# Kernel optimization log

Measured on AMD Instinct MI355X. Metric: run time of the kernel, lower is better.

Reference implementation:

```python
import jax, jax.numpy as jnp
import numpy as np

HEADS = 4
CHANNEL = 96
SCALE = CHANNEL ** (-0.5)


def setup_inputs() -> dict:
    key = jax.random.key(0)
    ks = jax.random.split(key, 6)
    x = jax.random.normal(ks[0], (64, 96, 112, 112), dtype=jnp.float32)
    z = jax.random.normal(ks[1], (64, 6, 192), dtype=jnp.float32)
    Wq = jax.random.normal(ks[2], (192, HEADS * CHANNEL), dtype=jnp.float32) * 0.02
    bq = jax.random.normal(ks[3], (HEADS * CHANNEL,), dtype=jnp.float32) * 0.02
    Wo = jax.random.normal(ks[4], (HEADS * CHANNEL, 192), dtype=jnp.float32) * 0.02
    bo = jax.random.normal(ks[5], (192,), dtype=jnp.float32) * 0.02
    return {"x": x, "z": z, "Wq": Wq, "bq": bq, "Wo": Wo, "bo": bo}


def reference(x, z, Wq, bq, Wo, bo):
    b, c, h, w = x.shape
    _, m, d = z.shape
    # flatten spatial: (b, hw, c)
    xf = x.reshape(b, c, h * w).transpose(0, 2, 1)
    # q: (b, heads, m, c)
    q = (z @ Wq + bq).reshape(b, m, HEADS, c).transpose(0, 2, 1, 3)
    # scores: (b, heads, m, hw); K = V = xf shared across heads
    dots = jnp.einsum('bhmc,bnc->bhmn', q, xf) * SCALE
    attn = jax.nn.softmax(dots, axis=-1)
    out = jnp.einsum('bhmn,bnc->bhmc', attn, xf)
    # rearrange b h m c -> b m (h c)
    out = out.transpose(0, 2, 1, 3).reshape(b, m, HEADS * c)
    return z + out @ Wo + bo
```

## Files before the change

### kernel.cpp

```cpp
#include <hip/hip_runtime.h>

#define BB 64
#define NHEADS 4
#define MM 6
#define RR 24
#define CC 96
#define NN 12544
#define DD 192
#define NC 128
#define TCH 7
#define NGRP 14
#define QSCALE 0.10206207261596577f

typedef __attribute__((ext_vector_type(8))) short short8;
typedef __attribute__((ext_vector_type(4))) float float4v;

__device__ __forceinline__ ushort f2b(float f) {
    union { float f; unsigned int u; } v; v.f = f;
    unsigned int u = v.u;
    unsigned int r = (u + 0x7FFFu + ((u >> 16) & 1u)) >> 16;
    return (ushort)r;
}

__global__ __launch_bounds__(256) void kA(const float* __restrict__ z,
                                          const float* __restrict__ Wq,
                                          const float* __restrict__ bq,
                                          ushort* __restrict__ Qg,
                                          float* __restrict__ Oacc,
                                          float* __restrict__ sacc) {
    __shared__ float zl[MM * DD];
    int t = threadIdx.x;
    int b = blockIdx.x / 3;
    int rg = blockIdx.x % 3;
    for (int i = t; i < MM * DD; i += 256) zl[i] = z[(size_t)b * MM * DD + i];
    for (int i = t; i < 768; i += 256) Oacc[(size_t)b * RR * CC + rg * 768 + i] = 0.f;
    if (rg == 0 && t < RR) sacc[b * RR + t] = 0.f;
    __syncthreads();
    #pragma unroll
    for (int i = 0; i < 3; ++i) {
        int idx = t + i * 256;
        int rr = idx / CC;
        int ch = idx - rr * CC;
        int r = rg * 8 + rr;
        int h = r / MM, m = r - h * MM;
        int col = h * CC + ch;
        float acc = bq[col];
        #pragma unroll 4
        for (int k = 0; k < DD; ++k)
            acc += zl[m * DD + k] * Wq[(size_t)k * (NHEADS * CC) + col];
        Qg[((size_t)b * RR + r) * CC + ch] = f2b(acc * QSCALE);
    }
}

__global__ __launch_bounds__(256, 4) void kB(const float* __restrict__ x,
                                             const ushort* __restrict__ Qg,
                                             float* __restrict__ Oacc,
                                             float* __restrict__ sacc) {
    __shared__ ushort xs[CC * NC];
    __shared__ ushort es[32 * NC];
    __shared__ ushort Qs[32 * 104];
    __shared__ float sdenL[RR];

    int t = threadIdx.x;
    int b = blockIdx.x / NGRP;
    int grp = blockIdx.x - b * NGRP;
    int w = t >> 6, lane = t & 63, q = lane >> 4, l15 = lane & 15;

    for (int i = t; i < 32 * 104; i += 256) Qs[i] = 0;
    __syncthreads();
    for (int i = t; i < RR * CC; i += 256) {
        int r = i / CC, ch = i - r * CC;
        Qs[r * 104 + ch] = Qg[((size_t)b * RR + r) * CC + ch];
    }
    if (t < RR) sdenL[t] = 0.f;

    int rt2 = w & 1;
    int ct0 = (w >> 1) * 3;
    float4v oacc0 = {0.f,0.f,0.f,0.f}, oacc1 = {0.f,0.f,0.f,0.f}, oacc2 = {0.f,0.f,0.f,0.f};

    for (int c = 0; c < TCH; ++c) {
        int n0 = (grp * TCH + c) * NC;
        const float* xg = x + (size_t)b * CC * NN + n0;
        #pragma unroll
        for (int i = 0; i < 12; ++i) {
            int cc = t + i * 256;
            int ch = cc >> 5;
            int j4 = cc & 31;
            float4 v = *(const float4*)(xg + (size_t)ch * NN + j4 * 4);
            ushort4 wv;
            wv.x = f2b(v.x); wv.y = f2b(v.y); wv.z = f2b(v.z); wv.w = f2b(v.w);
            int phys = (j4 >> 1) ^ (ch & 7);
            *(ushort4*)(&xs[ch * NC + phys * 8 + (j4 & 1) * 4]) = wv;
        }
        __syncthreads();

        float4v s00 = {0.f,0.f,0.f,0.f}, s01 = {0.f,0.f,0.f,0.f};
        float4v s10 = {0.f,0.f,0.f,0.f}, s11 = {0.f,0.f,0.f,0.f};
        #pragma unroll
        for (int kt = 0; kt < 3; ++kt) {
            short8 bf0, bf1;
            #pragma unroll
            for (int ntj = 0; ntj < 2; ++ntj) {
                int n = (2 * w + ntj) * 16 + l15;
                int chunkL = n >> 3, nin = n & 7;
                short8 bf;
                #pragma unroll
                for (int j = 0; j < 8; ++j) {
                    int R = kt * 32 + q * 8 + j;
                    bf[j] = (short)xs[R * NC + ((chunkL ^ j) << 3) + nin];
                }
                if (ntj == 0) bf0 = bf; else bf1 = bf;
            }
            short8 af0 = *(const short8*)(&Qs[(0 * 16 + l15) * 104 + kt * 32 + q * 8]);
            short8 af1 = *(const short8*)(&Qs[(1 * 16 + l15) * 104 + kt * 32 + q * 8]);
            s00 = __builtin_amdgcn_mfma_f32_16x16x32_bf16(af0, bf0, s00, 0, 0, 0);
            s01 = __builtin_amdgcn_mfma_f32_16x16x32_bf16(af0, bf1, s01, 0, 0, 0);
            s10 = __builtin_amdgcn_mfma_f32_16x16x32_bf16(af1, bf0, s10, 0, 0, 0);
            s11 = __builtin_amdgcn_mfma_f32_16x16x32_bf16(af1, bf1, s11, 0, 0, 0);
        }
        #pragma unroll
        for (int rt = 0; rt < 2; ++rt) {
            #pragma unroll
            for (int ntj = 0; ntj < 2; ++ntj) {
                float4v sv = rt == 0 ? (ntj == 0 ? s00 : s01) : (ntj == 0 ? s10 : s11);
                int n = (2 * w + ntj) * 16 + l15;
                int chunkL = n >> 3, nin = n & 7;
                #pragma unroll
                for (int reg = 0; reg < 4; ++reg) {
                    int r = rt * 16 + q * 4 + reg;
                    float e = __expf(fminf(fmaxf(sv[reg], -30.f), 30.f));
                    es[r * NC + (((chunkL ^ (r & 7))) << 3) + nin] = f2b(e);
                    if (r < RR) atomicAdd(&sdenL[r], e);
                }
            }
        }
        __syncthreads();

        #pragma unroll
        for (int kt = 0; kt < 4; ++kt) {
            int kbase = kt * 32 + q * 8;
            int chunkL = kbase >> 3;
            int ar = rt2 * 16 + l15;
            short8 af = *(const short8*)(&es[ar * NC + ((chunkL ^ (ar & 7)) << 3)]);
            int cr0 = (ct0 + 0) * 16 + l15;
            int cr1 = (ct0 + 1) * 16 + l15;
            int cr2 = (ct0 + 2) * 16 + l15;
            short8 b0 = *(const short8*)(&xs[cr0 * NC + ((chunkL ^ (cr0 & 7)) << 3)]);
            short8 b1 = *(const short8*)(&xs[cr1 * NC + ((chunkL ^ (cr1 & 7)) << 3)]);
            short8 b2 = *(const short8*)(&xs[cr2 * NC + ((chunkL ^ (cr2 & 7)) << 3)]);
            oacc0 = __builtin_amdgcn_mfma_f32_16x16x32_bf16(af, b0, oacc0, 0, 0, 0);
            oacc1 = __builtin_amdgcn_mfma_f32_16x16x32_bf16(af, b1, oacc1, 0, 0, 0);
            oacc2 = __builtin_amdgcn_mfma_f32_16x16x32_bf16(af, b2, oacc2, 0, 0, 0);
        }
        __syncthreads();
    }

    if (t < RR) atomicAdd(&sacc[b * RR + t], sdenL[t]);
    #pragma unroll
    for (int reg = 0; reg < 4; ++reg) {
        int r = rt2 * 16 + q * 4 + reg;
        if (r < RR) {
            size_t base = ((size_t)b * RR + r) * CC + l15;
            atomicAdd(&Oacc[base + (ct0 + 0) * 16], oacc0[reg]);
            atomicAdd(&Oacc[base + (ct0 + 1) * 16], oacc1[reg]);
            atomicAdd(&Oacc[base + (ct0 + 2) * 16], oacc2[reg]);
        }
    }
}

__global__ __launch_bounds__(192) void kC(const float* __restrict__ z,
                                          const float* __restrict__ Wo,
                                          const float* __restrict__ bo,
                                          const float* __restrict__ Oacc,
                                          const float* __restrict__ sacc,
                                          float* __restrict__ out) {
    __shared__ float oh[NHEADS * CC];
    int t = threadIdx.x;
    int b = blockIdx.x / MM;
    int m = blockIdx.x - b * MM;
    for (int i = t; i < NHEADS * CC; i += 192) {
        int h = i / CC, ch = i - h * CC;
        int r = h * MM + m;
        oh[i] = Oacc[((size_t)b * RR + r) * CC + ch] / sacc[b * RR + r];
    }
    __syncthreads();
    int d = t;
    float acc = bo[d] + z[((size_t)b * MM + m) * DD + d];
    #pragma unroll 8
    for (int k = 0; k < NHEADS * CC; ++k)
        acc += oh[k] * Wo[(size_t)k * DD + d];
    out[((size_t)b * MM + m) * DD + d] = acc;
}

extern "C" void kernel_launch(void* const* d_in, const int* in_sizes, int n_in,
                              void* d_out, int out_size, void* d_ws, size_t ws_size,
                              hipStream_t stream) {
    const float* x  = (const float*)d_in[0];
    const float* z  = (const float*)d_in[1];
    const float* Wq = (const float*)d_in[2];
    const float* bq = (const float*)d_in[3];
    const float* Wo = (const float*)d_in[4];
    const float* bo = (const float*)d_in[5];

    ushort* Qg  = (ushort*)d_ws;
    float* Oacc = (float*)((char*)d_ws + 294912);
    float* sacc = (float*)((char*)d_ws + 294912 + 589824);

    kA<<<BB * 3, 256, 0, stream>>>(z, Wq, bq, Qg, Oacc, sacc);
    kB<<<BB * NGRP, 256, 0, stream>>>(x, Qg, Oacc, sacc);
    kC<<<BB * MM, 192, 0, stream>>>(z, Wo, bo, Oacc, sacc, (float*)d_out);
}
```

Baseline: 603.3 us.

## Prefetch next x tile into registers, split work finer, and drop shared atomics

Global loads of the next x chunk are issued into registers before the score MFMAs, so the HBM reads overlap compute. Each block now handles 2 chunks instead of 7, across 49 blocks per batch, which gives more parallelism. The per-element shared-memory atomicAdd for the softmax denominator is replaced by per-thread partial sums, wave shuffles and a per-wave shared buffer. The padded rows 24-31 are trimmed with clamped indices, and a new swizzle function is used. The cost is more global atomics on Oacc and more register pressure from the 12 float4 prefetch registers.

```diff
diff --git a/kernel.cpp b/kernel.cpp
--- a/kernel.cpp
+++ b/kernel.cpp
@@ -8,8 +8,8 @@
 #define NN 12544
 #define DD 192
 #define NC 128
-#define TCH 7
-#define NGRP 14
+#define TCH 2
+#define NBLK 49
 #define QSCALE 0.10206207261596577f
 
 typedef __attribute__((ext_vector_type(8))) short short8;
@@ -21,6 +21,7 @@
     unsigned int r = (u + 0x7FFFu + ((u >> 16) & 1u)) >> 16;
     return (ushort)r;
 }
+__device__ __forceinline__ int swz(int row) { return (row ^ (row >> 3)) & 7; }
 
 __global__ __launch_bounds__(256) void kA(const float* __restrict__ z,
                                           const float* __restrict__ Wq,
@@ -57,42 +58,60 @@
                                              float* __restrict__ Oacc,
                                              float* __restrict__ sacc) {
     __shared__ ushort xs[CC * NC];
-    __shared__ ushort es[32 * NC];
-    __shared__ ushort Qs[32 * 104];
-    __shared__ float sdenL[RR];
+    __shared__ ushort es[RR * NC];
+    __shared__ ushort Qs[RR * 104];
+    __shared__ float sdenW[4 * RR];
 
     int t = threadIdx.x;
-    int b = blockIdx.x / NGRP;
-    int grp = blockIdx.x - b * NGRP;
+    int b = blockIdx.x / NBLK;
+    int blk = blockIdx.x - b * NBLK;
     int w = t >> 6, lane = t & 63, q = lane >> 4, l15 = lane & 15;
 
-    for (int i = t; i < 32 * 104; i += 256) Qs[i] = 0;
-    __syncthreads();
+    const float* xgb = x + (size_t)b * CC * NN + (size_t)blk * TCH * NC;
+
+    int sch[12], sj4[12];
+    #pragma unroll
+    for (int i = 0; i < 12; ++i) {
+        int cc = t + i * 256;
+        sch[i] = cc >> 5;
+        sj4[i] = cc & 31;
+    }
+
+    float4 pf[12];
+    #pragma unroll
+    for (int i = 0; i < 12; ++i)
+        pf[i] = *(const float4*)(xgb + (size_t)sch[i] * NN + sj4[i] * 4);
+
     for (int i = t; i < RR * CC; i += 256) {
         int r = i / CC, ch = i - r * CC;
-        Qs[r * 104 + ch] = Qg[((size_t)b * RR + r) * CC + ch];
-    }
-    if (t < RR) sdenL[t] = 0.f;
+        Qs[r * 104 + ch] = Qg[(size_t)b * RR * CC + i];
+    }
 
     int rt2 = w & 1;
     int ct0 = (w >> 1) * 3;
     float4v oacc0 = {0.f,0.f,0.f,0.f}, oacc1 = {0.f,0.f,0.f,0.f}, oacc2 = {0.f,0.f,0.f,0.f};
+    float pden[8] = {0.f,0.f,0.f,0.f,0.f,0.f,0.f,0.f};
+
+    int qr0 = l15;
+    int qr1 = (16 + l15 > 23) ? 23 : 16 + l15;
 
     for (int c = 0; c < TCH; ++c) {
-        int n0 = (grp * TCH + c) * NC;
-        const float* xg = x + (size_t)b * CC * NN + n0;
         #pragma unroll
         for (int i = 0; i < 12; ++i) {
-            int cc = t + i * 256;
-            int ch = cc >> 5;
-            int j4 = cc & 31;
-            float4 v = *(const float4*)(xg + (size_t)ch * NN + j4 * 4);
             ushort4 wv;
-            wv.x = f2b(v.x); wv.y = f2b(v.y); wv.z = f2b(v.z); wv.w = f2b(v.w);
-            int phys = (j4 >> 1) ^ (ch & 7);
-            *(ushort4*)(&xs[ch * NC + phys * 8 + (j4 & 1) * 4]) = wv;
+            wv.x = f2b(pf[i].x); wv.y = f2b(pf[i].y);
+            wv.z = f2b(pf[i].z); wv.w = f2b(pf[i].w);
+            int phys = (sj4[i] >> 1) ^ swz(sch[i]);
+            *(ushort4*)(&xs[sch[i] * NC + phys * 8 + (sj4[i] & 1) * 4]) = wv;
         }
         __syncthreads();
+
+        if (c + 1 < TCH) {
+            const float* xg = xgb + (size_t)(c + 1) * NC;
+            #pragma unroll
+            for (int i = 0; i < 12; ++i)
+                pf[i] = *(const float4*)(xg + (size_t)sch[i] * NN + sj4[i] * 4);
+        }
 
         float4v s00 = {0.f,0.f,0.f,0.f}, s01 = {0.f,0.f,0.f,0.f};
         float4v s10 = {0.f,0.f,0.f,0.f}, s11 = {0.f,0.f,0.f,0.f};
@@ -102,52 +121,54 @@
             #pragma unroll
             for (int ntj = 0; ntj < 2; ++ntj) {
                 int n = (2 * w + ntj) * 16 + l15;
-                int chunkL = n >> 3, nin = n & 7;
+                int chL = n >> 3, nin = n & 7;
                 short8 bf;
                 #pragma unroll
                 for (int j = 0; j < 8; ++j) {
                     int R = kt * 32 + q * 8 + j;
-                    bf[j] = (short)xs[R * NC + ((chunkL ^ j) << 3) + nin];
+                    bf[j] = (short)xs[R * NC + ((chL ^ swz(R)) << 3) + nin];
                 }
                 if (ntj == 0) bf0 = bf; else bf1 = bf;
             }
-            short8 af0 = *(const short8*)(&Qs[(0 * 16 + l15) * 104 + kt * 32 + q * 8]);
-            short8 af1 = *(const short8*)(&Qs[(1 * 16 + l15) * 104 + kt * 32 + q * 8]);
+            short8 af0 = *(const short8*)(&Qs[qr0 * 104 + kt * 32 + q * 8]);
+            short8 af1 = *(const short8*)(&Qs[qr1 * 104 + kt * 32 + q * 8]);
             s00 = __builtin_amdgcn_mfma_f32_16x16x32_bf16(af0, bf0, s00, 0, 0, 0);
             s01 = __builtin_amdgcn_mfma_f32_16x16x32_bf16(af0, bf1, s01, 0, 0, 0);
             s10 = __builtin_amdgcn_mfma_f32_16x16x32_bf16(af1, bf0, s10, 0, 0, 0);
             s11 = __builtin_amdgcn_mfma_f32_16x16x32_bf16(af1, bf1, s11, 0, 0, 0);
         }
+
         #pragma unroll
         for (int rt = 0; rt < 2; ++rt) {
             #pragma unroll
             for (int ntj = 0; ntj < 2; ++ntj) {
                 float4v sv = rt == 0 ? (ntj == 0 ? s00 : s01) : (ntj == 0 ? s10 : s11);
                 int n = (2 * w + ntj) * 16 + l15;
-                int chunkL = n >> 3, nin = n & 7;
+                int chLn = n >> 3, nin = n & 7;
                 #pragma unroll
                 for (int reg = 0; reg < 4; ++reg) {
                     int r = rt * 16 + q * 4 + reg;
-                    float e = __expf(fminf(fmaxf(sv[reg], -30.f), 30.f));
-                    es[r * NC + (((chunkL ^ (r & 7))) << 3) + nin] = f2b(e);
-                    if (r < RR) atomicAdd(&sdenL[r], e);
+                    if (r < RR) {
+                        float e = __expf(fminf(fmaxf(sv[reg], -30.f), 30.f));
+                        es[r * NC + ((chLn ^ swz(r)) << 3) + nin] = f2b(e);
+                        pden[rt * 4 + reg] += e;
+                    }
                 }
             }
         }
         __syncthreads();
 
+        int ar = rt2 * 16 + l15; if (ar > 23) ar = 23;
+        int cr0 = (ct0 + 0) * 16 + l15;
+        int cr1 = (ct0 + 1) * 16 + l15;
+        int cr2 = (ct0 + 2) * 16 + l15;
         #pragma unroll
         for (int kt = 0; kt < 4; ++kt) {
-            int kbase = kt * 32 + q * 8;
-            int chunkL = kbase >> 3;
-            int ar = rt2 * 16 + l15;
-            short8 af = *(const short8*)(&es[ar * NC + ((chunkL ^ (ar & 7)) << 3)]);
-            int cr0 = (ct0 + 0) * 16 + l15;
-            int cr1 = (ct0 + 1) * 16 + l15;
-            int cr2 = (ct0 + 2) * 16 + l15;
-            short8 b0 = *(const short8*)(&xs[cr0 * NC + ((chunkL ^ (cr0 & 7)) << 3)]);
-            short8 b1 = *(const short8*)(&xs[cr1 * NC + ((chunkL ^ (cr1 & 7)) << 3)]);
-            short8 b2 = *(const short8*)(&xs[cr2 * NC + ((chunkL ^ (cr2 & 7)) << 3)]);
+            int chL = kt * 4 + q;
+            short8 af = *(const short8*)(&es[ar * NC + ((chL ^ swz(ar)) << 3)]);
+            short8 b0 = *(const short8*)(&xs[cr0 * NC + ((chL ^ swz(cr0)) << 3)]);
+            short8 b1 = *(const short8*)(&xs[cr1 * NC + ((chL ^ swz(cr1)) << 3)]);
+            short8 b2 = *(const short8*)(&xs[cr2 * NC + ((chL ^ swz(cr2)) << 3)]);
             oacc0 = __builtin_amdgcn_mfma_f32_16x16x32_bf16(af, b0, oacc0, 0, 0, 0);
             oacc1 = __builtin_amdgcn_mfma_f32_16x16x32_bf16(af, b1, oacc1, 0, 0, 0);
             oacc2 = __builtin_amdgcn_mfma_f32_16x16x32_bf16(af, b2, oacc2, 0, 0, 0);
@@ -155,7 +176,22 @@
         __syncthreads();
     }
 
-    if (t < RR) atomicAdd(&sacc[b * RR + t], sdenL[t]);
+    #pragma unroll
+    for (int rt = 0; rt < 2; ++rt) {
+        #pragma unroll
+        for (int reg = 0; reg < 4; ++reg) {
+            float v = pden[rt * 4 + reg];
+            v += __shfl_xor(v, 1, 64); v += __shfl_xor(v, 2, 64);
+            v += __shfl_xor(v, 4, 64); v += __shfl_xor(v, 8, 64);
+            int row = rt * 16 + q * 4 + reg;
+            if (l15 == 0 && row < RR) sdenW[w * RR + row] = v;
+        }
+    }
+    __syncthreads();
+    if (t < RR)
+        atomicAdd(&sacc[b * RR + t],
+                  sdenW[t] + sdenW[RR + t] + sdenW[2 * RR + t] + sdenW[3 * RR + t]);
+
     #pragma unroll
     for (int reg = 0; reg < 4; ++reg) {
         int r = rt2 * 16 + q * 4 + reg;
@@ -207,6 +243,6 @@
     float* sacc = (float*)((char*)d_ws + 294912 + 589824);
 
     kA<<<BB * 3, 256, 0, stream>>>(z, Wq, bq, Qg, Oacc, sacc);
-    kB<<<BB * NGRP, 256, 0, stream>>>(x, Qg, Oacc, sacc);
+    kB<<<BB * NBLK, 256, 0, stream>>>(x, Qg, Oacc, sacc);
     kC<<<BB * MM, 192, 0, stream>>>(z, Wo, bo, Oacc, sacc, (float*)d_out);
 }
```

Result: slower. 639.8 us (+6.1%).
